# Performance work log

Hardware: AMD Instinct MI355X
Metric: run time of the kernel (lower is better)

## Reference

```python
import jax, jax.numpy as jnp
import numpy as np

B, S, D, H = 2, 2048, 1024, 16
HD = D // H  # 64

def _make_freqs():
    # flux-style rotation matrices: [1,1,S,HD//2,2,2]
    theta = 10000.0
    inv = 1.0 / (theta ** (np.arange(0, HD, 2, dtype=np.float32) / HD))  # [HD//2]
    pos = np.arange(S, dtype=np.float32)
    ang = pos[:, None] * inv[None, :]  # [S, HD//2]
    cos, sin = np.cos(ang), np.sin(ang)
    rot = np.stack([np.stack([cos, -sin], -1), np.stack([sin, cos], -1)], -2)  # [S,HD//2,2,2]
    return jnp.asarray(rot[None, None], dtype=jnp.float32)

def setup_inputs() -> dict:
    key = jax.random.key(0)
    ks = jax.random.split(key, 9)
    sc = 1.0 / np.sqrt(D)
    return {
        "x": jax.random.normal(ks[0], (B, S, D), jnp.float32),
        "freqs": _make_freqs(),
        "Wq": jax.random.normal(ks[1], (D, D), jnp.float32) * sc,
        "bq": jax.random.normal(ks[2], (D,), jnp.float32) * 0.01,
        "Wk": jax.random.normal(ks[3], (D, D), jnp.float32) * sc,
        "bk": jax.random.normal(ks[4], (D,), jnp.float32) * 0.01,
        "Wv": jax.random.normal(ks[5], (D, D), jnp.float32) * sc,
        "bv": jax.random.normal(ks[6], (D,), jnp.float32) * 0.01,
        "Wo": jax.random.normal(ks[7], (D, D), jnp.float32) * sc,
        "bo": jax.random.normal(ks[8], (D,), jnp.float32) * 0.01,
    }

def _apply_rope(xq, xk, freqs):
    # xq/xk: [B,H,S,HD]; freqs: [1,1,S,HD//2,2,2]
    def rot(t):
        t_ = t.reshape(*t.shape[:-1], -1, 1, 2)  # [B,H,S,HD//2,1,2]
        out = freqs[..., 0] * t_[..., 0] + freqs[..., 1] * t_[..., 1]  # [B,H,S,HD//2,2]
        return out.reshape(t.shape).astype(t.dtype)
    return rot(xq), rot(xk)

def reference(x, freqs, Wq, bq, Wk, bk, Wv, bv, Wo, bo):
    b, s, _ = x.shape
    # QKV projections (torch Linear: x @ W.T + b)
    q = (x @ Wq.T + bq).reshape(b, s, H, HD).transpose(0, 2, 1, 3)  # [B,H,S,HD]
    k = (x @ Wk.T + bk).reshape(b, s, H, HD).transpose(0, 2, 1, 3)
    v = (x @ Wv.T + bv).reshape(b, s, H, HD).transpose(0, 2, 1, 3)
    q, k = _apply_rope(q, k, freqs)
    # scaled dot product attention, no mask, no dropout
    scale = 1.0 / jnp.sqrt(jnp.asarray(HD, x.dtype))
    scores = jnp.einsum("bhqd,bhkd->bhqk", q, k) * scale
    attn = jax.nn.softmax(scores, axis=-1)
    o = jnp.einsum("bhqk,bhkd->bhqd", attn, v)  # [B,H,S,HD]
    o = o.transpose(0, 2, 1, 3).reshape(b, s, D)
    return o @ Wo.T + bo
```

## Files before the change

kernel.cpp:

```cpp
#include <hip/hip_runtime.h>
#include <cmath>

#define B_ 2
#define S_ 2048
#define D_ 1024
#define H_ 16
#define HD_ 64
#define M_ 4096

typedef __attribute__((ext_vector_type(8))) short short8;
typedef __attribute__((ext_vector_type(4))) short short4v;
typedef __attribute__((ext_vector_type(4))) float f32x4;

__device__ __forceinline__ short f2bf(float x) {
    unsigned u = __builtin_bit_cast(unsigned, x);
    u += 0x7fffu + ((u >> 16) & 1u);
    return (short)(u >> 16);
}

__device__ __forceinline__ void gload_lds16(const short* g, short* l) {
    __builtin_amdgcn_global_load_lds(
        (const __attribute__((address_space(1))) unsigned int*)g,
        (__attribute__((address_space(3))) unsigned int*)l, 16, 0, 0);
}

__global__ __launch_bounds__(256) void cast_all_kernel(
    const float* __restrict__ x,  const float* __restrict__ Wq,
    const float* __restrict__ Wk, const float* __restrict__ Wv,
    const float* __restrict__ Wo,
    short* __restrict__ xb, short* __restrict__ Wqkvb, short* __restrict__ Wob)
{
    const size_t i = (size_t)blockIdx.x * 256 + threadIdx.x;
    const float* src; short* dst; size_t off;
    if (i < 1048576)      { src = x;  dst = xb;              off = i; }
    else if (i < 1310720) { src = Wq; dst = Wqkvb;           off = i - 1048576; }
    else if (i < 1572864) { src = Wk; dst = Wqkvb + 1048576; off = i - 1310720; }
    else if (i < 1835008) { src = Wv; dst = Wqkvb + 2097152; off = i - 1572864; }
    else                  { src = Wo; dst = Wob;             off = i - 1835008; }
    float4 v = ((const float4*)src)[off];
    short4v o = { f2bf(v.x), f2bf(v.y), f2bf(v.z), f2bf(v.w) };
    ((short4v*)dst)[off] = o;
}

template<int MODE, int TM, int TN>
__global__ __launch_bounds__(256) void gemm_mfma(
    const short* __restrict__ A, const short* __restrict__ Bw,
    const float* __restrict__ b0p, const float* __restrict__ b1p, const float* __restrict__ b2p,
    const float* __restrict__ freqs,
    void* __restrict__ out0, void* __restrict__ out1, void* __restrict__ out2)
{
    constexpr int RT = TM / 32, CT = TN / 32;
    __shared__ __align__(16) short As[2][TM*32];
    __shared__ __align__(16) short Bs[2][TN*32];
    const int t = threadIdx.x;
    const int w = t >> 6;
    const int lane = t & 63;
    const int qd = lane >> 4, l = lane & 15;
    const int n0 = blockIdx.x * TN, m0 = blockIdx.y * TM;
    const int wr = (w >> 1) * (TM/2), wc = (w & 1) * (TN/2);
    const int srow = lane >> 2;
    const int scol = (lane & 3) * 8;

    #define STAGE(buf, k0)                                                         \
        do {                                                                       \
            _Pragma("unroll")                                                      \
            for (int j = 0; j < TM/64; ++j) {                                      \
                const int rr = (j*4 + w) * 16;                                     \
                gload_lds16(A  + (size_t)(m0 + rr + srow)*1024 + (k0) + scol,      \
                            &As[buf][rr*32]);                                      \
            }                                                                      \
            _Pragma("unroll")                                                      \
            for (int j = 0; j < TN/64; ++j) {                                      \
                const int rr = (j*4 + w) * 16;                                     \
                gload_lds16(Bw + (size_t)(n0 + rr + srow)*1024 + (k0) + scol,      \
                            &Bs[buf][rr*32]);                                      \
            }                                                                      \
        } while (0)

    f32x4 acc[RT][CT] = {};
    STAGE(0, 0);

    for (int k0 = 0; k0 < 1024; k0 += 32) {
        const int cur = (k0 >> 5) & 1;
        __syncthreads();
        if (k0 + 32 < 1024) STAGE(cur ^ 1, k0 + 32);
        short8 af[RT], bf[CT];
        #pragma unroll
        for (int rt = 0; rt < RT; ++rt)
            af[rt] = *(const short8*)&As[cur][(wr + rt*16 + l)*32 + qd*8];
        #pragma unroll
        for (int ct = 0; ct < CT; ++ct)
            bf[ct] = *(const short8*)&Bs[cur][(wc + ct*16 + l)*32 + qd*8];
        #pragma unroll
        for (int rt = 0; rt < RT; ++rt)
            #pragma unroll
            for (int ct = 0; ct < CT; ++ct)
                acc[rt][ct] = __builtin_amdgcn_mfma_f32_16x16x32_bf16(af[rt], bf[ct], acc[rt][ct], 0, 0, 0);
    }
    #undef STAGE

    if (MODE == 0) {
        float* out = (float*)out0;
        #pragma unroll
        for (int rt = 0; rt < RT; ++rt)
            #pragma unroll
            for (int ct = 0; ct < CT; ++ct) {
                const int n = n0 + wc + ct*16 + l;
                const float bias = b0p[n];
                #pragma unroll
                for (int r = 0; r < 4; ++r) {
                    const int m = m0 + wr + rt*16 + qd*4 + r;
                    out[(size_t)m*1024 + n] = acc[rt][ct][r] + bias;
                }
            }
    } else {
        const int sel = n0 >> 10;
        const int nb = n0 & 1023;
        const float* bias = (sel == 0) ? b0p : (sel == 1) ? b1p : b2p;
        if (sel < 2) {
            short* outg = (short*)((sel == 0) ? out0 : out1);
            #pragma unroll
            for (int rt = 0; rt < RT; ++rt)
                #pragma unroll
                for (int ct = 0; ct < CT; ++ct) {
                    const int d = nb + wc + ct*16 + l;
                    const float bsv = bias[d];
                    const int h = d >> 6, hd = d & 63;
                    #pragma unroll
                    for (int r = 0; r < 4; ++r) {
                        const int m = m0 + wr + rt*16 + qd*4 + r;
                        const int bb = m >> 11, s = m & 2047;
                        float val = acc[rt][ct][r] + bsv;
                        float pv = __shfl_xor(val, 1);
                        const float* f = freqs + (size_t)s*128 + (size_t)(hd >> 1)*4;
                        float o = (d & 1) ? (f[2]*pv + f[3]*val) : (f[0]*val + f[1]*pv);
                        outg[((size_t)(bb*16 + h)*2048 + s)*64 + hd] = f2bf(o);
                    }
                }
        } else {
            short* outv = (short*)out2;
            #pragma unroll
            for (int rt = 0; rt < RT; ++rt)
                #pragma unroll
                for (int ct = 0; ct < CT; ++ct) {
                    const int d = nb + wc + ct*16 + l;
                    const float bsv = bias[d];
                    const int h = d >> 6, hd = d & 63;
                    const int m0r = m0 + wr + rt*16 + qd*4;
                    const int bb = m0r >> 11, s0 = m0r & 2047;
                    short4v pk;
                    #pragma unroll
                    for (int r = 0; r < 4; ++r) pk[r] = f2bf(acc[rt][ct][r] + bsv);
                    *(short4v*)&outv[((size_t)(bb*16 + h)*64 + hd)*2048 + s0] = pk;
                }
        }
    }
}

__global__ __launch_bounds__(256) void attn_mfma(
    const short* __restrict__ qg, const short* __restrict__ kg,
    const short* __restrict__ vtg, short* __restrict__ og)
{
    __shared__ __align__(16) short KP[128*136];
    __shared__ __align__(16) short Vt[64*136];

    const int t = threadIdx.x;
    const int w = t >> 6;
    const int lane = t & 63;
    const int qd = lane >> 4, l = lane & 15;
    const int q0 = blockIdx.x * 128;
    const int bh = blockIdx.y;

    short8 qf[2][2];
    const short* qb = qg + ((size_t)bh*2048 + q0 + w*32)*64;
    #pragma unroll
    for (int rt = 0; rt < 2; ++rt)
        #pragma unroll
        for (int kf = 0; kf < 2; ++kf)
            qf[rt][kf] = *(const short8*)&qb[(rt*16 + l)*64 + kf*32 + qd*8];

    f32x4 oacc[2][4] = {};
    float lsum[2] = {};

    const short* kbase = kg  + (size_t)bh*2048*64;
    const short* vbase = vtg + (size_t)bh*64*2048;
    const float SC = 0.125f * 1.44269504088896340736f;

    for (int kt = 0; kt < 16; ++kt) {
        __syncthreads();
        {
            const short* src = kbase + (size_t)(kt*128 + (t>>1))*64 + (t&1)*32;
            short* dst = &KP[(t>>1)*136 + (t&1)*32];
            *(short8*)(dst+0)  = *(const short8*)(src+0);
            *(short8*)(dst+8)  = *(const short8*)(src+8);
            *(short8*)(dst+16) = *(const short8*)(src+16);
            *(short8*)(dst+24) = *(const short8*)(src+24);
        }
        {
            const short* src = vbase + (size_t)(t>>2)*2048 + kt*128 + (t&3)*32;
            short* dst = &Vt[(t>>2)*136 + (t&3)*32];
            *(short8*)(dst+0)  = *(const short8*)(src+0);
            *(short8*)(dst+8)  = *(const short8*)(src+8);
            *(short8*)(dst+16) = *(const short8*)(src+16);
            *(short8*)(dst+24) = *(const short8*)(src+24);
        }
        __syncthreads();

        f32x4 sacc[2][8] = {};
        #pragma unroll
        for (int ct = 0; ct < 8; ++ct) {
            short8 k0f = *(const short8*)&KP[(ct*16 + l)*136 + qd*8];
            short8 k1f = *(const short8*)&KP[(ct*16 + l)*136 + 32 + qd*8];
            #pragma unroll
            for (int rt = 0; rt < 2; ++rt) {
                sacc[rt][ct] = __builtin_amdgcn_mfma_f32_16x16x32_bf16(k0f, qf[rt][0], sacc[rt][ct], 0, 0, 0);
                sacc[rt][ct] = __builtin_amdgcn_mfma_f32_16x16x32_bf16(k1f, qf[rt][1], sacc[rt][ct], 0, 0, 0);
            }
        }
        __syncthreads();

        #pragma unroll
        for (int rt = 0; rt < 2; ++rt)
            #pragma unroll
            for (int ct = 0; ct < 8; ++ct) {
                short4v pk;
                #pragma unroll
                for (int r = 0; r < 4; ++r) {
                    float p = exp2f(sacc[rt][ct][r] * SC);
                    lsum[rt] += p;
                    pk[r] = f2bf(p);
                }
                *(short4v*)&KP[(w*32 + rt*16 + l)*136 + ct*16 + qd*4] = pk;
            }

        #pragma unroll
        for (int kf = 0; kf < 4; ++kf) {
            short8 pa0 = *(const short8*)&KP[(w*32 +  0 + l)*136 + kf*32 + qd*8];
            short8 pa1 = *(const short8*)&KP[(w*32 + 16 + l)*136 + kf*32 + qd*8];
            #pragma unroll
            for (int ht = 0; ht < 4; ++ht) {
                short8 vb = *(const short8*)&Vt[(ht*16 + l)*136 + kf*32 + qd*8];
                oacc[0][ht] = __builtin_amdgcn_mfma_f32_16x16x32_bf16(pa0, vb, oacc[0][ht], 0, 0, 0);
                oacc[1][ht] = __builtin_amdgcn_mfma_f32_16x16x32_bf16(pa1, vb, oacc[1][ht], 0, 0, 0);
            }
        }
    }

    #pragma unroll
    for (int rt = 0; rt < 2; ++rt) {
        lsum[rt] += __shfl_xor(lsum[rt], 16);
        lsum[rt] += __shfl_xor(lsum[rt], 32);
    }
    float inv[2][4];
    #pragma unroll
    for (int rt = 0; rt < 2; ++rt)
        #pragma unroll
        for (int r = 0; r < 4; ++r)
            inv[rt][r] = 1.0f / __shfl(lsum[rt], qd*4 + r);

    const int bb = bh >> 4, h = bh & 15;
    #pragma unroll
    for (int rt = 0; rt < 2; ++rt)
        #pragma unroll
        for (int ht = 0; ht < 4; ++ht)
            #pragma unroll
            for (int r = 0; r < 4; ++r) {
                const int s = q0 + w*32 + rt*16 + qd*4 + r;
                og[((size_t)bb*2048 + s)*1024 + h*64 + ht*16 + l] =
                    f2bf(oacc[rt][ht][r] * inv[rt][r]);
            }
}

extern "C" void kernel_launch(void* const* d_in, const int* in_sizes, int n_in,
                              void* d_out, int out_size, void* d_ws, size_t ws_size,
                              hipStream_t stream)
{
    const float* x  = (const float*)d_in[0];
    const float* fr = (const float*)d_in[1];
    const float* Wq = (const float*)d_in[2];
    const float* bq = (const float*)d_in[3];
    const float* Wk = (const float*)d_in[4];
    const float* bk = (const float*)d_in[5];
    const float* Wv = (const float*)d_in[6];
    const float* bv = (const float*)d_in[7];
    const float* Wo = (const float*)d_in[8];
    const float* bo = (const float*)d_in[9];
    float* out = (float*)d_out;

    short* ws    = (short*)d_ws;
    short* xb    = ws;
    short* Wqkvb = xb    + 4194304;
    short* Wob   = Wqkvb + 3145728;
    short* qg    = Wob   + 1048576;
    short* kg    = qg    + 4194304;
    short* vtg   = kg    + 4194304;
    short* og    = vtg   + 4194304;

    cast_all_kernel<<<8192, 256, 0, stream>>>(x, Wq, Wk, Wv, Wo, xb, Wqkvb, Wob);
    gemm_mfma<1,128,128><<<dim3(24, 32), 256, 0, stream>>>(xb, Wqkvb, bq, bk, bv, fr, qg, kg, vtg);
    attn_mfma<<<dim3(16, 32), 256, 0, stream>>>(qg, kg, vtg, og);
    gemm_mfma<0,64,64><<<dim3(16, 64), 256, 0, stream>>>(og, Wob, bo, nullptr, nullptr, nullptr,
                                                         out, nullptr, nullptr);
}
```

Before: 282.3 us.

## Replace LDS-staged GEMM with direct global-to-register fragment loads

Both projection GEMMs drop the shared-memory double buffer filled through global_load_lds and the per-step __syncthreads. Each wave now loads its MFMA fragments straight from global memory into registers, double-buffered in registers across k-steps. This removes LDS traffic and block-wide barriers. In exchange, operands are no longer shared between the waves of a block, so more global and L2 traffic is needed and the 16-byte per-lane row-strided loads are less well coalesced.

```diff
diff --git a/kernel.cpp b/kernel.cpp
--- a/kernel.cpp
+++ b/kernel.cpp
@@ -16,12 +16,6 @@
     unsigned u = __builtin_bit_cast(unsigned, x);
     u += 0x7fffu + ((u >> 16) & 1u);
     return (short)(u >> 16);
-}
-
-__device__ __forceinline__ void gload_lds16(const short* g, short* l) {
-    __builtin_amdgcn_global_load_lds(
-        (const __attribute__((address_space(1))) unsigned int*)g,
-        (__attribute__((address_space(3))) unsigned int*)l, 16, 0, 0);
 }
 
 __global__ __launch_bounds__(256) void cast_all_kernel(
@@ -42,62 +36,56 @@
     ((short4v*)dst)[off] = o;
 }
 
-template<int MODE, int TM, int TN>
-__global__ __launch_bounds__(256) void gemm_mfma(
+template<int MODE, int WM, int WN>
+__global__ __launch_bounds__(256) void gemm_direct(
     const short* __restrict__ A, const short* __restrict__ Bw,
     const float* __restrict__ b0p, const float* __restrict__ b1p, const float* __restrict__ b2p,
     const float* __restrict__ freqs,
     void* __restrict__ out0, void* __restrict__ out1, void* __restrict__ out2)
 {
-    constexpr int RT = TM / 32, CT = TN / 32;
-    __shared__ __align__(16) short As[2][TM*32];
-    __shared__ __align__(16) short Bs[2][TN*32];
+    constexpr int RT = WM / 16, CT = WN / 16;
     const int t = threadIdx.x;
     const int w = t >> 6;
     const int lane = t & 63;
     const int qd = lane >> 4, l = lane & 15;
-    const int n0 = blockIdx.x * TN, m0 = blockIdx.y * TM;
-    const int wr = (w >> 1) * (TM/2), wc = (w & 1) * (TN/2);
-    const int srow = lane >> 2;
-    const int scol = (lane & 3) * 8;
-
-    #define STAGE(buf, k0)                                                         \
+    const int n0 = blockIdx.x * (2*WN), m0 = blockIdx.y * (2*WM);
+    const int wr = (w >> 1) * WM, wc = (w & 1) * WN;
+
+    const short* Ab = A  + (size_t)(m0 + wr)*1024 + qd*8;
+    const short* Bb = Bw + (size_t)(n0 + wc)*1024 + qd*8;
+
+    short8 fa[2][RT], fb[2][CT];
+    f32x4 acc[RT][CT] = {};
+
+    #define LOAD(buf, koff)                                                        \
         do {                                                                       \
             _Pragma("unroll")                                                      \
-            for (int j = 0; j < TM/64; ++j) {                                      \
-                const int rr = (j*4 + w) * 16;                                     \
-                gload_lds16(A  + (size_t)(m0 + rr + srow)*1024 + (k0) + scol,      \
-                            &As[buf][rr*32]);                                      \
-            }                                                                      \
+            for (int rt = 0; rt < RT; ++rt)                                        \
+                fa[buf][rt] = *(const short8*)(Ab + (size_t)(rt*16 + l)*1024 + (koff)); \
             _Pragma("unroll")                                                      \
-            for (int j = 0; j < TN/64; ++j) {                                      \
-                const int rr = (j*4 + w) * 16;                                     \
-                gload_lds16(Bw + (size_t)(n0 + rr + srow)*1024 + (k0) + scol,      \
-                            &Bs[buf][rr*32]);                                      \
-            }                                                                      \
+            for (int ct = 0; ct < CT; ++ct)                                        \
+                fb[buf][ct] = *(const short8*)(Bb + (size_t)(ct*16 + l)*1024 + (koff)); \
         } while (0)
 
-    f32x4 acc[RT][CT] = {};
-    STAGE(0, 0);
-
-    for (int k0 = 0; k0 < 1024; k0 += 32) {
-        const int cur = (k0 >> 5) & 1;
-        __syncthreads();
-        if (k0 + 32 < 1024) STAGE(cur ^ 1, k0 + 32);
-        short8 af[RT], bf[CT];
-        #pragma unroll
-        for (int rt = 0; rt < RT; ++rt)
-            af[rt] = *(const short8*)&As[cur][(wr + rt*16 + l)*32 + qd*8];
-        #pragma unroll
-        for (int ct = 0; ct < CT; ++ct)
-            bf[ct] = *(const short8*)&Bs[cur][(wc + ct*16 + l)*32 + qd*8];
-        #pragma unroll
-        for (int rt = 0; rt < RT; ++rt)
-            #pragma unroll
-            for (int ct = 0; ct < CT; ++ct)
-                acc[rt][ct] = __builtin_amdgcn_mfma_f32_16x16x32_bf16(af[rt], bf[ct], acc[rt][ct], 0, 0, 0);
-    }
-    #undef STAGE
+    #define MM(buf)                                                                \
+        do {                                                                       \
+            _Pragma("unroll")                                                      \
+            for (int rt = 0; rt < RT; ++rt)                                        \
+                _Pragma("unroll")                                                  \
+                for (int ct = 0; ct < CT; ++ct)                                    \
+                    acc[rt][ct] = __builtin_amdgcn_mfma_f32_16x16x32_bf16(         \
+                        fa[buf][rt], fb[buf][ct], acc[rt][ct], 0, 0, 0);           \
+        } while (0)
+
+    LOAD(0, 0);
+    for (int k0 = 0; k0 < 1024; k0 += 64) {
+        LOAD(1, k0 + 32);
+        MM(0);
+        if (k0 + 64 < 1024) LOAD(0, k0 + 64);
+        MM(1);
+    }
+    #undef LOAD
+    #undef MM
 
     if (MODE == 0) {
         float* out = (float*)out0;
@@ -297,8 +285,8 @@
     short* og    = vtg   + 4194304;
 
     cast_all_kernel<<<8192, 256, 0, stream>>>(x, Wq, Wk, Wv, Wo, xb, Wqkvb, Wob);
-    gemm_mfma<1,128,128><<<dim3(24, 32), 256, 0, stream>>>(xb, Wqkvb, bq, bk, bv, fr, qg, kg, vtg);
+    gemm_direct<1,64,64><<<dim3(24, 32), 256, 0, stream>>>(xb, Wqkvb, bq, bk, bv, fr, qg, kg, vtg);
     attn_mfma<<<dim3(16, 32), 256, 0, stream>>>(qg, kg, vtg, og);
-    gemm_mfma<0,64,64><<<dim3(16, 64), 256, 0, stream>>>(og, Wob, bo, nullptr, nullptr, nullptr,
-                                                         out, nullptr, nullptr);
-}
+    gemm_direct<0,32,32><<<dim3(16, 64), 256, 0, stream>>>(og, Wob, bo, nullptr, nullptr, nullptr,
+                                                           out, nullptr, nullptr);
+}
```

Result: slower. 378.3 us (+34.0%).

## Drop GEMM double buffering and read attention K/V directly from global memory

Applied to the files above, without the earlier changes.

The GEMM kernel now uses a single LDS buffer with a load-then-sync per k-step instead of double-buffered prefetch, and the QKV projection tile shrinks from 128x128 to 128x64 so twice as many blocks launch. The attention kernel no longer stages K and V tiles cooperatively in shared memory. Each wave reads its K and V fragments straight from global memory and keeps only a private LDS slice for the P matrix. This removes block-wide barriers and LDS traffic, but it exposes global-load latency in the GEMM and makes each wave fetch the same K/V data again, relying on cache.

```diff
diff --git a/kernel.cpp b/kernel.cpp
--- a/kernel.cpp
+++ b/kernel.cpp
@@ -43,15 +43,15 @@
 }
 
 template<int MODE, int TM, int TN>
-__global__ __launch_bounds__(256) void gemm_mfma(
+__global__ __launch_bounds__(256) void gemm_tile(
     const short* __restrict__ A, const short* __restrict__ Bw,
     const float* __restrict__ b0p, const float* __restrict__ b1p, const float* __restrict__ b2p,
     const float* __restrict__ freqs,
     void* __restrict__ out0, void* __restrict__ out1, void* __restrict__ out2)
 {
     constexpr int RT = TM / 32, CT = TN / 32;
-    __shared__ __align__(16) short As[2][TM*32];
-    __shared__ __align__(16) short Bs[2][TN*32];
+    __shared__ __align__(16) short As[TM*32];
+    __shared__ __align__(16) short Bs[TN*32];
     const int t = threadIdx.x;
     const int w = t >> 6;
     const int lane = t & 63;
@@ -61,43 +61,34 @@
     const int srow = lane >> 2;
     const int scol = (lane & 3) * 8;
 
-    #define STAGE(buf, k0)                                                         \
-        do {                                                                       \
-            _Pragma("unroll")                                                      \
-            for (int j = 0; j < TM/64; ++j) {                                      \
-                const int rr = (j*4 + w) * 16;                                     \
-                gload_lds16(A  + (size_t)(m0 + rr + srow)*1024 + (k0) + scol,      \
-                            &As[buf][rr*32]);                                      \
-            }                                                                      \
-            _Pragma("unroll")                                                      \
-            for (int j = 0; j < TN/64; ++j) {                                      \
-                const int rr = (j*4 + w) * 16;                                     \
-                gload_lds16(Bw + (size_t)(n0 + rr + srow)*1024 + (k0) + scol,      \
-                            &Bs[buf][rr*32]);                                      \
-            }                                                                      \
-        } while (0)
-
     f32x4 acc[RT][CT] = {};
-    STAGE(0, 0);
 
     for (int k0 = 0; k0 < 1024; k0 += 32) {
-        const int cur = (k0 >> 5) & 1;
         __syncthreads();
-        if (k0 + 32 < 1024) STAGE(cur ^ 1, k0 + 32);
+        #pragma unroll
+        for (int j = 0; j < TM/64; ++j) {
+            const int rr = (j*4 + w) * 16;
+            gload_lds16(A + (size_t)(m0 + rr + srow)*1024 + k0 + scol, &As[rr*32]);
+        }
+        #pragma unroll
+        for (int j = 0; j < TN/64; ++j) {
+            const int rr = (j*4 + w) * 16;
+            gload_lds16(Bw + (size_t)(n0 + rr + srow)*1024 + k0 + scol, &Bs[rr*32]);
+        }
+        __syncthreads();
         short8 af[RT], bf[CT];
         #pragma unroll
         for (int rt = 0; rt < RT; ++rt)
-            af[rt] = *(const short8*)&As[cur][(wr + rt*16 + l)*32 + qd*8];
+            af[rt] = *(const short8*)&As[(wr + rt*16 + l)*32 + qd*8];
         #pragma unroll
         for (int ct = 0; ct < CT; ++ct)
-            bf[ct] = *(const short8*)&Bs[cur][(wc + ct*16 + l)*32 + qd*8];
+            bf[ct] = *(const short8*)&Bs[(wc + ct*16 + l)*32 + qd*8];
         #pragma unroll
         for (int rt = 0; rt < RT; ++rt)
             #pragma unroll
             for (int ct = 0; ct < CT; ++ct)
                 acc[rt][ct] = __builtin_amdgcn_mfma_f32_16x16x32_bf16(af[rt], bf[ct], acc[rt][ct], 0, 0, 0);
     }
-    #undef STAGE
 
     if (MODE == 0) {
         float* out = (float*)out0;
@@ -161,8 +152,7 @@
     const short* __restrict__ qg, const short* __restrict__ kg,
     const short* __restrict__ vtg, short* __restrict__ og)
 {
-    __shared__ __align__(16) short KP[128*136];
-    __shared__ __align__(16) short Vt[64*136];
+    __shared__ __align__(16) short Ps[4][32*136];
 
     const int t = threadIdx.x;
     const int w = t >> 6;
@@ -170,6 +160,7 @@
     const int qd = lane >> 4, l = lane & 15;
     const int q0 = blockIdx.x * 128;
     const int bh = blockIdx.y;
+    short* myP = &Ps[w][0];
 
     short8 qf[2][2];
     const short* qb = qg + ((size_t)bh*2048 + q0 + w*32)*64;
@@ -187,37 +178,19 @@
     const float SC = 0.125f * 1.44269504088896340736f;
 
     for (int kt = 0; kt < 16; ++kt) {
-        __syncthreads();
-        {
-            const short* src = kbase + (size_t)(kt*128 + (t>>1))*64 + (t&1)*32;
-            short* dst = &KP[(t>>1)*136 + (t&1)*32];
-            *(short8*)(dst+0)  = *(const short8*)(src+0);
-            *(short8*)(dst+8)  = *(const short8*)(src+8);
-            *(short8*)(dst+16) = *(const short8*)(src+16);
-            *(short8*)(dst+24) = *(const short8*)(src+24);
-        }
-        {
-            const short* src = vbase + (size_t)(t>>2)*2048 + kt*128 + (t&3)*32;
-            short* dst = &Vt[(t>>2)*136 + (t&3)*32];
-            *(short8*)(dst+0)  = *(const short8*)(src+0);
-            *(short8*)(dst+8)  = *(const short8*)(src+8);
-            *(short8*)(dst+16) = *(const short8*)(src+16);
-            *(short8*)(dst+24) = *(const short8*)(src+24);
-        }
-        __syncthreads();
+        const short* kt_p = kbase + (size_t)kt*128*64;
 
         f32x4 sacc[2][8] = {};
         #pragma unroll
         for (int ct = 0; ct < 8; ++ct) {
-            short8 k0f = *(const short8*)&KP[(ct*16 + l)*136 + qd*8];
-            short8 k1f = *(const short8*)&KP[(ct*16 + l)*136 + 32 + qd*8];
+            short8 ka = *(const short8*)(kt_p + (size_t)(ct*16 + l)*64 + qd*8);
+            short8 kb = *(const short8*)(kt_p + (size_t)(ct*16 + l)*64 + 32 + qd*8);
             #pragma unroll
             for (int rt = 0; rt < 2; ++rt) {
-                sacc[rt][ct] = __builtin_amdgcn_mfma_f32_16x16x32_bf16(k0f, qf[rt][0], sacc[rt][ct], 0, 0, 0);
-                sacc[rt][ct] = __builtin_amdgcn_mfma_f32_16x16x32_bf16(k1f, qf[rt][1], sacc[rt][ct], 0, 0, 0);
-            }
-        }
-        __syncthreads();
+                sacc[rt][ct] = __builtin_amdgcn_mfma_f32_16x16x32_bf16(ka, qf[rt][0], sacc[rt][ct], 0, 0, 0);
+                sacc[rt][ct] = __builtin_amdgcn_mfma_f32_16x16x32_bf16(kb, qf[rt][1], sacc[rt][ct], 0, 0, 0);
+            }
+        }
 
         #pragma unroll
         for (int rt = 0; rt < 2; ++rt)
@@ -230,18 +203,18 @@
                     lsum[rt] += p;
                     pk[r] = f2bf(p);
                 }
-                *(short4v*)&KP[(w*32 + rt*16 + l)*136 + ct*16 + qd*4] = pk;
+                *(short4v*)&myP[(rt*16 + l)*136 + ct*16 + qd*4] = pk;
             }
 
         #pragma unroll
         for (int kf = 0; kf < 4; ++kf) {
-            short8 pa0 = *(const short8*)&KP[(w*32 +  0 + l)*136 + kf*32 + qd*8];
-            short8 pa1 = *(const short8*)&KP[(w*32 + 16 + l)*136 + kf*32 + qd*8];
+            short8 pa0 = *(const short8*)&myP[( 0 + l)*136 + kf*32 + qd*8];
+            short8 pa1 = *(const short8*)&myP[(16 + l)*136 + kf*32 + qd*8];
             #pragma unroll
             for (int ht = 0; ht < 4; ++ht) {
-                short8 vb = *(const short8*)&Vt[(ht*16 + l)*136 + kf*32 + qd*8];
-                oacc[0][ht] = __builtin_amdgcn_mfma_f32_16x16x32_bf16(pa0, vb, oacc[0][ht], 0, 0, 0);
-                oacc[1][ht] = __builtin_amdgcn_mfma_f32_16x16x32_bf16(pa1, vb, oacc[1][ht], 0, 0, 0);
+                short8 vv = *(const short8*)(vbase + (size_t)(ht*16 + l)*2048 + kt*128 + kf*32 + qd*8);
+                oacc[0][ht] = __builtin_amdgcn_mfma_f32_16x16x32_bf16(pa0, vv, oacc[0][ht], 0, 0, 0);
+                oacc[1][ht] = __builtin_amdgcn_mfma_f32_16x16x32_bf16(pa1, vv, oacc[1][ht], 0, 0, 0);
             }
         }
     }
@@ -297,8 +270,8 @@
     short* og    = vtg   + 4194304;
 
     cast_all_kernel<<<8192, 256, 0, stream>>>(x, Wq, Wk, Wv, Wo, xb, Wqkvb, Wob);
-    gemm_mfma<1,128,128><<<dim3(24, 32), 256, 0, stream>>>(xb, Wqkvb, bq, bk, bv, fr, qg, kg, vtg);
+    gemm_tile<1,128,64><<<dim3(48, 32), 256, 0, stream>>>(xb, Wqkvb, bq, bk, bv, fr, qg, kg, vtg);
     attn_mfma<<<dim3(16, 32), 256, 0, stream>>>(qg, kg, vtg, og);
-    gemm_mfma<0,64,64><<<dim3(16, 64), 256, 0, stream>>>(og, Wob, bo, nullptr, nullptr, nullptr,
+    gemm_tile<0,64,64><<<dim3(16, 64), 256, 0, stream>>>(og, Wob, bo, nullptr, nullptr, nullptr,
                                                          out, nullptr, nullptr);
 }
```

Measured after the change: 326.0 us. +15.5%, slower.

## Replace double-buffered GEMM k-loop with 128-wide chunked loads and narrower QKV tiles

Applied to the files above, without the earlier changes.

The GEMM mainloop no longer double-buffers 32-wide k-slices. It now loads a 128-wide k-chunk (four sub-slices) into LDS, synchronises, and runs four MFMA steps before loading the next chunk. This cuts the number of barriers per k-loop, but load and compute no longer overlap inside a block. The QKV projection also changes tile shape from 128x128 to 128x64, doubling the grid to raise block count and occupancy.

```diff
diff --git a/kernel.cpp b/kernel.cpp
--- a/kernel.cpp
+++ b/kernel.cpp
@@ -43,15 +43,15 @@
 }
 
 template<int MODE, int TM, int TN>
-__global__ __launch_bounds__(256) void gemm_mfma(
+__global__ __launch_bounds__(256) void gemm_chunk(
     const short* __restrict__ A, const short* __restrict__ Bw,
     const float* __restrict__ b0p, const float* __restrict__ b1p, const float* __restrict__ b2p,
     const float* __restrict__ freqs,
     void* __restrict__ out0, void* __restrict__ out1, void* __restrict__ out2)
 {
     constexpr int RT = TM / 32, CT = TN / 32;
-    __shared__ __align__(16) short As[2][TM*32];
-    __shared__ __align__(16) short Bs[2][TN*32];
+    __shared__ __align__(16) short As[4*TM*32];
+    __shared__ __align__(16) short Bs[4*TN*32];
     const int t = threadIdx.x;
     const int w = t >> 6;
     const int lane = t & 63;
@@ -61,43 +61,42 @@
     const int srow = lane >> 2;
     const int scol = (lane & 3) * 8;
 
-    #define STAGE(buf, k0)                                                         \
-        do {                                                                       \
-            _Pragma("unroll")                                                      \
-            for (int j = 0; j < TM/64; ++j) {                                      \
-                const int rr = (j*4 + w) * 16;                                     \
-                gload_lds16(A  + (size_t)(m0 + rr + srow)*1024 + (k0) + scol,      \
-                            &As[buf][rr*32]);                                      \
-            }                                                                      \
-            _Pragma("unroll")                                                      \
-            for (int j = 0; j < TN/64; ++j) {                                      \
-                const int rr = (j*4 + w) * 16;                                     \
-                gload_lds16(Bw + (size_t)(n0 + rr + srow)*1024 + (k0) + scol,      \
-                            &Bs[buf][rr*32]);                                      \
-            }                                                                      \
-        } while (0)
-
     f32x4 acc[RT][CT] = {};
-    STAGE(0, 0);
-
-    for (int k0 = 0; k0 < 1024; k0 += 32) {
-        const int cur = (k0 >> 5) & 1;
-        __syncthreads();
-        if (k0 + 32 < 1024) STAGE(cur ^ 1, k0 + 32);
-        short8 af[RT], bf[CT];
-        #pragma unroll
-        for (int rt = 0; rt < RT; ++rt)
-            af[rt] = *(const short8*)&As[cur][(wr + rt*16 + l)*32 + qd*8];
-        #pragma unroll
-        for (int ct = 0; ct < CT; ++ct)
-            bf[ct] = *(const short8*)&Bs[cur][(wc + ct*16 + l)*32 + qd*8];
-        #pragma unroll
-        for (int rt = 0; rt < RT; ++rt)
+
+    for (int k0 = 0; k0 < 1024; k0 += 128) {
+        __syncthreads();
+        #pragma unroll
+        for (int sub = 0; sub < 4; ++sub) {
+            #pragma unroll
+            for (int j = 0; j < TM/64; ++j) {
+                const int rr = (j*4 + w) * 16;
+                gload_lds16(A + (size_t)(m0 + rr + srow)*1024 + k0 + sub*32 + scol,
+                            &As[sub*TM*32 + rr*32]);
+            }
+            #pragma unroll
+            for (int j = 0; j < TN/64; ++j) {
+                const int rr = (j*4 + w) * 16;
+                gload_lds16(Bw + (size_t)(n0 + rr + srow)*1024 + k0 + sub*32 + scol,
+                            &Bs[sub*TN*32 + rr*32]);
+            }
+        }
+        __syncthreads();
+        #pragma unroll
+        for (int sub = 0; sub < 4; ++sub) {
+            short8 af[RT], bf[CT];
+            #pragma unroll
+            for (int rt = 0; rt < RT; ++rt)
+                af[rt] = *(const short8*)&As[sub*TM*32 + (wr + rt*16 + l)*32 + qd*8];
             #pragma unroll
             for (int ct = 0; ct < CT; ++ct)
-                acc[rt][ct] = __builtin_amdgcn_mfma_f32_16x16x32_bf16(af[rt], bf[ct], acc[rt][ct], 0, 0, 0);
+                bf[ct] = *(const short8*)&Bs[sub*TN*32 + (wc + ct*16 + l)*32 + qd*8];
+            #pragma unroll
+            for (int rt = 0; rt < RT; ++rt)
+                #pragma unroll
+                for (int ct = 0; ct < CT; ++ct)
+                    acc[rt][ct] = __builtin_amdgcn_mfma_f32_16x16x32_bf16(af[rt], bf[ct], acc[rt][ct], 0, 0, 0);
+        }
     }
-    #undef STAGE
 
     if (MODE == 0) {
         float* out = (float*)out0;
@@ -297,8 +296,8 @@
     short* og    = vtg   + 4194304;
 
     cast_all_kernel<<<8192, 256, 0, stream>>>(x, Wq, Wk, Wv, Wo, xb, Wqkvb, Wob);
-    gemm_mfma<1,128,128><<<dim3(24, 32), 256, 0, stream>>>(xb, Wqkvb, bq, bk, bv, fr, qg, kg, vtg);
+    gemm_chunk<1,128,64><<<dim3(48, 32), 256, 0, stream>>>(xb, Wqkvb, bq, bk, bv, fr, qg, kg, vtg);
     attn_mfma<<<dim3(16, 32), 256, 0, stream>>>(qg, kg, vtg, og);
-    gemm_mfma<0,64,64><<<dim3(16, 64), 256, 0, stream>>>(og, Wob, bo, nullptr, nullptr, nullptr,
-                                                         out, nullptr, nullptr);
-}
+    gemm_chunk<0,64,64><<<dim3(16, 64), 256, 0, stream>>>(og, Wob, bo, nullptr, nullptr, nullptr,
+                                                          out, nullptr, nullptr);
+}
```

Result: faster. 248.7 us (-11.9%).
